# Kernel optimization log

Hardware: AMD Instinct MI355X
Metric: run time of the kernel (lower is better)

Reference implementation:

```python
import jax, jax.numpy as jnp
import numpy as np

B, N, IN_CH = 4, 8192, 4
K = 16
W0, W1, W2 = 64, 128, 256
NUM_CLASSES = 3


def setup_inputs() -> dict:
    key = jax.random.key(0)
    ks = jax.random.split(key, 16)

    def lin(kw, kb, fan_in, fan_out):
        bound = 1.0 / np.sqrt(fan_in)
        w = jax.random.uniform(kw, (fan_in, fan_out), jnp.float32, -bound, bound)
        b = jax.random.uniform(kb, (fan_out,), jnp.float32, -bound, bound)
        return w, b

    x = jax.random.normal(ks[0], (B, N, IN_CH), jnp.float32)
    stem_w, stem_b = lin(ks[1], ks[2], IN_CH, W0)
    b1_w, b1_b = lin(ks[3], ks[4], 2 * W0 + 3, W1)
    b2_w, b2_b = lin(ks[5], ks[6], 2 * W1 + 3, W2)
    glob_w, glob_b = lin(ks[7], ks[8], W2, W2)
    head1_w, head1_b = lin(ks[9], ks[10], 2 * W2, W2)
    head2_w, head2_b = lin(ks[11], ks[12], W2, NUM_CLASSES)
    return {
        'x': x,
        'hmix_a': jnp.float32(1.0), 'hmix_b': jnp.float32(1.0), 'hmix_c': jnp.float32(0.0),
        'stem_w': stem_w, 'stem_b': stem_b,
        'b1_w': b1_w, 'b1_b': b1_b,
        'b2_w': b2_w, 'b2_b': b2_b,
        'glob_w': glob_w, 'glob_b': glob_b,
        'head1_w': head1_w, 'head1_b': head1_b,
        'head2_w': head2_w, 'head2_b': head2_b,
        'thresh': jnp.float32(0.15), 'sharp': jnp.float32(10.0), 'scale': jnp.float32(0.5),
    }


def _knn_idx(coords, k):
    # coords: [B,N,3] -> idx of k nearest neighbors (incl. self), no grad.
    c = jax.lax.stop_gradient(coords)
    xx = jnp.sum(c * c, axis=-1, keepdims=True)            # [B,N,1]
    dist = xx + jnp.swapaxes(xx, 1, 2) - 2.0 * jnp.einsum('bnc,bmc->bnm', c, c)
    dist = jnp.maximum(dist, 0.0)
    _, idx = jax.lax.top_k(-dist, k)                       # smallest distances
    return idx                                             # [B,N,k]


def _local_agg(coords, feat, idx, w, b):
    # gather-concat-MLP-maxpool, faithful to LocalAggBlock (pool='max')
    bidx = jnp.arange(coords.shape[0])[:, None, None]
    nb_f = feat[bidx, idx]                                 # [B,N,k,C]
    nb_p = coords[bidx, idx]                               # [B,N,k,3]
    fi = feat[:, :, None, :]
    pi = coords[:, :, None, :]
    h = jnp.concatenate(
        [jnp.broadcast_to(fi, nb_f.shape), nb_f - fi, nb_p - pi], axis=-1)
    h = jax.nn.relu(jnp.einsum('bnkd,do->bnko', h, w) + b)
    return jnp.max(h, axis=2)                              # [B,N,out]


def reference(x, hmix_a, hmix_b, hmix_c, stem_w, stem_b, b1_w, b1_b,
              b2_w, b2_b, glob_w, glob_b, head1_w, head1_b,
              head2_w, head2_b, thresh, sharp, scale):
    # HeightMixer: z_eff = a*z + b*hag + c
    z_eff = hmix_a * x[..., 2] + hmix_b * x[..., 3] + hmix_c
    coords = jnp.stack([x[..., 0], x[..., 1], z_eff], axis=-1)  # [B,N,3]

    f = jax.nn.relu(x @ stem_w + stem_b)                   # stem: [B,N,64]

    # both blocks use the same coords -> same KNN graph; compute once
    idx = _knn_idx(coords, K)
    f = _local_agg(coords, f, idx, b1_w, b1_b)             # [B,N,128]
    f = _local_agg(coords, f, idx, b2_w, b2_b)             # [B,N,256]

    g = jnp.max(f, axis=1)                                 # [B,256]
    g = jax.nn.relu(g @ glob_w + glob_b)
    g = jnp.broadcast_to(g[:, None, :], f.shape)           # [B,N,256]

    h = jnp.concatenate([f, g], axis=-1)                   # [B,N,512]
    h = jax.nn.relu(h @ head1_w + head1_b)
    logits = h @ head2_w + head2_b                         # [B,N,3]

    # HeightPriorBias on class 0
    hag = x[..., 3]
    bias = scale * jax.nn.sigmoid(sharp * (thresh - hag))
    logits = logits.at[..., 0].add(bias)
    return logits
```

## Files before the change

### kernel.cpp

```cpp
#include <hip/hip_runtime.h>
#include <math.h>

typedef unsigned long long u64;
typedef unsigned int u32;
typedef _Float16 h8v __attribute__((ext_vector_type(8)));
typedef float    f4v __attribute__((ext_vector_type(4)));
typedef float    f2v __attribute__((ext_vector_type(2)));

#define MFMA16(a,b,c) __builtin_amdgcn_mfma_f32_16x16x32_f16(a, b, c, 0, 0, 0)

#define B_ 4
#define N_ 8192
#define K_ 16
#define W0_ 64
#define W1_ 128
#define W2_ 256
#define X0_ 96
#define X1_ 160

__global__ __launch_bounds__(256) void prep_kernel(
    const float* __restrict__ x,
    const float* __restrict__ stem_w, const float* __restrict__ stem_b,
    const float* __restrict__ hmix_a, const float* __restrict__ hmix_b,
    const float* __restrict__ hmix_c,
    float* __restrict__ coords4, _Float16* __restrict__ fx0,
    _Float16* __restrict__ fx1) {
  const int p = blockIdx.x * 4 + (threadIdx.x >> 6);
  const int o = threadIdx.x & 63;
  const float x0 = x[p*4+0], x1 = x[p*4+1], x2 = x[p*4+2], x3 = x[p*4+3];
  const float z = hmix_a[0]*x2 + hmix_b[0]*x3 + hmix_c[0];
  float acc = stem_b[o] + x0*stem_w[0*W0_+o] + x1*stem_w[1*W0_+o]
            + x2*stem_w[2*W0_+o] + x3*stem_w[3*W0_+o];
  fx0[p*X0_+o] = (_Float16)fmaxf(acc, 0.f);
  if (o < 32) {
    const float tv = (o==0) ? x0 : (o==1) ? x1 : (o==2) ? z : 0.f;
    fx0[p*X0_+W0_+o] = (_Float16)tv;
    fx1[(size_t)p*X1_+W1_+o] = (_Float16)tv;
  }
  if (o == 0) {
    const float xx = x0*x0 + x1*x1 + z*z;
    ((float4*)coords4)[p] = make_float4(x0, x1, z, xx);
  }
}

template<int DIN, int DOUT, int XDIM>
__global__ void wconv_kernel(const float* __restrict__ w,
    _Float16* __restrict__ midT, _Float16* __restrict__ difT) {
  const int o = blockIdx.x;
  const int c = threadIdx.x;
  float mv = 0.f, dv = 0.f;
  if (c < DIN)        { const float wm = w[(DIN+c)*DOUT+o]; mv = wm; dv = w[c*DOUT+o] - wm; }
  else if (c < DIN+3) { const float wp = w[(2*DIN+(c-DIN))*DOUT+o]; mv = wp; dv = -wp; }
  midT[o*XDIM+c] = (_Float16)mv;
  difT[o*XDIM+c] = (_Float16)dv;
}

__global__ __launch_bounds__(256) void htrans_kernel(
    const float* __restrict__ h1w, _Float16* __restrict__ h1wT) {
  const int o = blockIdx.x;
  for (int c = threadIdx.x; c < 512; c += 256)
    h1wT[(size_t)o*512 + c] = (_Float16)h1w[(size_t)c*256 + o];
}

#define DPP_SHR1(v) __builtin_amdgcn_update_dpp(0, (v), 0x138, 0xF, 0xF, false)

#define DPP_MIN(v, ctrl)                                                        \
  { const int _t = __builtin_amdgcn_update_dpp(__float_as_int(v),               \
      __float_as_int(v), ctrl, 0xF, 0xF, false);                                \
    v = fminf(v, __int_as_float(_t)); }

__device__ __forceinline__ float sixteenth_of_minima(float v) {
  float th = 0.f;
#pragma unroll
  for (int r = 0; r < 16; ++r) {
    float w = v;
    DPP_MIN(w, 0x111); DPP_MIN(w, 0x112); DPP_MIN(w, 0x114); DPP_MIN(w, 0x118);
    DPP_MIN(w, 0x142); DPP_MIN(w, 0x143);
    const float mv = __int_as_float(
        __builtin_amdgcn_readlane(__float_as_int(w), 63));
    th = mv;
    v = (v == mv) ? INFINITY : v;
  }
  return th;
}

#define KNN_EVT(d, dk, ik)                                                      \
  {                                                                             \
    const int s = (int)__ffsll((unsigned long long)m) - 1;  m &= m - 1;         \
    const float dc = __int_as_float(__builtin_amdgcn_readlane(                  \
                       __float_as_int(d), s));                                  \
    const bool cnd = dc < dk;                                                   \
    const u64 cm = __ballot(cnd) << 1;                                          \
    const float pd = __int_as_float(DPP_SHR1(__float_as_int(dk)));              \
    const int   pi = DPP_SHR1(ik);                                              \
    const bool pc = (cm >> lane) & 1;                                           \
    dk = cnd ? (pc ? pd : dc) : dk;                                             \
    ik = cnd ? (pc ? pi : (jbase + s)) : ik;                                    \
  }

#define KNN_CHUNK(d, dk, ik, T, Th)                                             \
  { u64 m = __ballot(d <= T);                                                   \
    if (m) {                                                                    \
      do { KNN_EVT(d, dk, ik) } while (m);                                      \
      T = fminf(Th, __int_as_float(__builtin_amdgcn_readlane(                   \
            __float_as_int(dk), 15)));                                          \
    }                                                                           \
  }

#define KNN_DIST2(dA, dB)                                                       \
  const f2v cjx = {cj.x, cj.x}, cjy = {cj.y, cj.y},                             \
            cjz = {cj.z, cj.z}, cjw = {cj.w, cj.w};                             \
  f2v tA = cAx * cjx;                                                           \
  tA = __builtin_elementwise_fma(cAy, cjy, tA);                                 \
  tA = __builtin_elementwise_fma(cAz, cjz, tA);                                 \
  const f2v dA = __builtin_elementwise_fma(tA, m2, cAw + cjw);                  \
  f2v tB = cBx * cjx;                                                           \
  tB = __builtin_elementwise_fma(cBy, cjy, tB);                                 \
  tB = __builtin_elementwise_fma(cBz, cjz, tB);                                 \
  const f2v dB = __builtin_elementwise_fma(tB, m2, cBw + cjw);

__global__ __launch_bounds__(256, 8) void knn_kernel(
    const float* __restrict__ coords4, int* __restrict__ knn_idx) {
  const int tid = threadIdx.x;
  const int wid = tid >> 6;
  const int lane = tid & 63;
  const int p0 = blockIdx.x * 16 + wid * 4;
  const int b = p0 >> 13;
  const float4* cb = ((const float4*)coords4) + (b << 13);
  const float4 c0 = ((const float4*)coords4)[p0+0];
  const float4 c1 = ((const float4*)coords4)[p0+1];
  const float4 c2 = ((const float4*)coords4)[p0+2];
  const float4 c3 = ((const float4*)coords4)[p0+3];
  const f2v m2 = {-2.f, -2.f};
  const f2v cAx = {c0.x, c1.x}, cAy = {c0.y, c1.y}, cAz = {c0.z, c1.z}, cAw = {c0.w, c1.w};
  const f2v cBx = {c2.x, c3.x}, cBy = {c2.y, c3.y}, cBz = {c2.z, c3.z}, cBw = {c2.w, c3.w};

  float lm0 = INFINITY, lm1 = INFINITY, lm2 = INFINITY, lm3 = INFINITY;
  for (int it = 0; it < 64; ++it) {
    const float4 cj = cb[it*64 + lane];
    KNN_DIST2(dA, dB)
    lm0 = fminf(lm0, fmaxf(dA[0], 0.f));
    lm1 = fminf(lm1, fmaxf(dA[1], 0.f));
    lm2 = fminf(lm2, fmaxf(dB[0], 0.f));
    lm3 = fminf(lm3, fmaxf(dB[1], 0.f));
  }
  const float Th0 = sixteenth_of_minima(lm0);
  const float Th1 = sixteenth_of_minima(lm1);
  const float Th2 = sixteenth_of_minima(lm2);
  const float Th3 = sixteenth_of_minima(lm3);

  float dk0 = INFINITY, dk1 = INFINITY, dk2 = INFINITY, dk3 = INFINITY;
  int   ik0 = 0, ik1 = 0, ik2 = 0, ik3 = 0;
  float T0 = Th0, T1 = Th1, T2 = Th2, T3 = Th3;

  for (int it = 0; it < N_/64; ++it) {
    const int jbase = it*64;
    const float4 cj = cb[jbase + lane];
    KNN_DIST2(dA, dB)
    const float d0 = fmaxf(dA[0], 0.f);
    const float d1 = fmaxf(dA[1], 0.f);
    const float d2 = fmaxf(dB[0], 0.f);
    const float d3 = fmaxf(dB[1], 0.f);
    KNN_CHUNK(d0, dk0, ik0, T0, Th0);
    KNN_CHUNK(d1, dk1, ik1, T1, Th1);
    KNN_CHUNK(d2, dk2, ik2, T2, Th2);
    KNN_CHUNK(d3, dk3, ik3, T3, Th3);
  }

  if (lane < K_) {
    knn_idx[(size_t)(p0+0)*K_ + lane] = ik0;
    knn_idx[(size_t)(p0+1)*K_ + lane] = ik1;
    knn_idx[(size_t)(p0+2)*K_ + lane] = ik2;
    knn_idx[(size_t)(p0+3)*K_ + lane] = ik3;
  }
}

template<int KS, int NPASS>
__global__ __launch_bounds__(256) void aggm_kernel(
    const _Float16* __restrict__ fx, const int* __restrict__ knn_idx,
    const _Float16* __restrict__ midT, const _Float16* __restrict__ difT,
    const float* __restrict__ bw,
    _Float16* __restrict__ fo, const int ostr) {
  const int XD  = KS*32;
  const int XDP = XD + 8;
  const int CH  = KS*4;
  const int p0 = blockIdx.x * 16;
  const int bb = (p0 >> 13) << 13;
  const int tid = threadIdx.x;
  const int w = tid >> 6, lane = tid & 63, col = lane & 15, quad = lane >> 4;
  const int koff = quad * 8;

  __shared__ int s_idx[256];
  __shared__ _Float16 sA[2][16*(KS*32+8)];

  s_idx[tid] = knn_idx[p0*K_ + tid];

  f4v cacc[NPASS][2];
  {
    h8v Ao[KS];
    const _Float16* ap = fx + (size_t)(p0+col)*XD + koff;
#pragma unroll
    for (int kk = 0; kk < KS; ++kk) Ao[kk] = *(const h8v*)(ap + kk*32);
#pragma unroll
    for (int ps = 0; ps < NPASS; ++ps) {
      const int o0 = ps*128 + w*32;
      const _Float16* b0 = difT + (size_t)(o0 + col)*XD + koff;
      const _Float16* b1 = difT + (size_t)(o0 + 16 + col)*XD + koff;
      f4v c0 = {0.f,0.f,0.f,0.f}, c1 = {0.f,0.f,0.f,0.f};
#pragma unroll
      for (int kk = 0; kk < KS; ++kk) {
        c0 = MFMA16(Ao[kk], *(const h8v*)(b0 + kk*32), c0);
        c1 = MFMA16(Ao[kk], *(const h8v*)(b1 + kk*32), c1);
      }
      cacc[ps][0] = c0; cacc[ps][1] = c1;
    }
  }

  h8v Bf[NPASS][2][KS];
  float bias[NPASS][2];
#pragma unroll
  for (int ps = 0; ps < NPASS; ++ps) {
    const int o0 = ps*128 + w*32;
#pragma unroll
    for (int kk = 0; kk < KS; ++kk) {
      Bf[ps][0][kk] = *(const h8v*)(midT + (size_t)(o0 + col)*XD + kk*32 + koff);
      Bf[ps][1][kk] = *(const h8v*)(midT + (size_t)(o0 + 16 + col)*XD + kk*32 + koff);
    }
    bias[ps][0] = bw[o0 + col];
    bias[ps][1] = bw[o0 + 16 + col];
  }
  __syncthreads();

  for (int c = tid; c < 16*CH; c += 256) {
    const int r = c / CH, o = c - r*CH;
    *(uint4*)&sA[0][r*XDP + o*8] =
        *(const uint4*)(fx + (size_t)(bb + s_idx[r<<4])*XD + o*8);
  }
  __syncthreads();

  f4v M[NPASS][2];
#pragma unroll
  for (int ps = 0; ps < NPASS; ++ps) {
    M[ps][0] = (f4v){-INFINITY,-INFINITY,-INFINITY,-INFINITY};
    M[ps][1] = (f4v){-INFINITY,-INFINITY,-INFINITY,-INFINITY};
  }

  for (int k = 0; k < 16; ++k) {
    const int buf = k & 1;
    if (k < 15) {
      for (int c = tid; c < 16*CH; c += 256) {
        const int r = c / CH, o = c - r*CH;
        *(uint4*)&sA[buf^1][r*XDP + o*8] =
            *(const uint4*)(fx + (size_t)(bb + s_idx[(r<<4) + k + 1])*XD + o*8);
      }
    }
    h8v Ac[KS];
    const _Float16* ap = &sA[buf][col*XDP + koff];
#pragma unroll
    for (int kk = 0; kk < KS; ++kk) Ac[kk] = *(const h8v*)(ap + kk*32);
#pragma unroll
    for (int ps = 0; ps < NPASS; ++ps) {
      f4v d0 = {0.f,0.f,0.f,0.f}, d1 = {0.f,0.f,0.f,0.f};
#pragma unroll
      for (int kk = 0; kk < KS; ++kk) {
        d0 = MFMA16(Ac[kk], Bf[ps][0][kk], d0);
        d1 = MFMA16(Ac[kk], Bf[ps][1][kk], d1);
      }
#pragma unroll
      for (int e = 0; e < 4; ++e) {
        M[ps][0][e] = fmaxf(M[ps][0][e], d0[e]);
        M[ps][1][e] = fmaxf(M[ps][1][e], d1[e]);
      }
    }
    __syncthreads();
  }

  const int prow = p0 + (quad << 2);
#pragma unroll
  for (int ps = 0; ps < NPASS; ++ps) {
    const int o0 = ps*128 + w*32;
    const int oa = o0 + col, ob = oa + 16;
#pragma unroll
    for (int reg = 0; reg < 4; ++reg) {
      fo[(size_t)(prow+reg)*ostr + oa] =
          (_Float16)fmaxf(M[ps][0][reg] + cacc[ps][0][reg] + bias[ps][0], 0.f);
      fo[(size_t)(prow+reg)*ostr + ob] =
          (_Float16)fmaxf(M[ps][1][reg] + cacc[ps][1][reg] + bias[ps][1], 0.f);
    }
  }
}

__global__ __launch_bounds__(256) void gmax_kernel(
    const _Float16* __restrict__ f2h, float* __restrict__ part) {
  const int b = blockIdx.x >> 5;
  const int seg = blockIdx.x & 31;
  const int tid = threadIdx.x;
  const int rg = tid >> 5;
  const int cc = (tid & 31) * 8;
  __shared__ float smax[8][256];
  const size_t rbase = (size_t)(b << 13) + seg*256;
  _Float16 mh[8];
#pragma unroll
  for (int j = 0; j < 8; ++j) mh[j] = (_Float16)0.f;
  for (int n = rg; n < 256; n += 8) {
    const h8v v = *(const h8v*)&f2h[(rbase + n)*W2_ + cc];
#pragma unroll
    for (int j = 0; j < 8; ++j) mh[j] = (v[j] > mh[j]) ? v[j] : mh[j];
  }
#pragma unroll
  for (int j = 0; j < 8; ++j) smax[rg][cc + j] = (float)mh[j];
  __syncthreads();
  float m = smax[0][tid];
#pragma unroll
  for (int g = 1; g < 8; ++g) m = fmaxf(m, smax[g][tid]);
  part[(size_t)blockIdx.x*W2_ + tid] = m;
}

__global__ __launch_bounds__(256) void gfc_kernel(
    const float* __restrict__ part, const float* __restrict__ gw,
    const float* __restrict__ gb, _Float16* __restrict__ g2h) {
  const int b = blockIdx.x;
  const int o = threadIdx.x;
  __shared__ float s_g[W2_];
  float m = -INFINITY;
  for (int s = 0; s < 32; ++s) m = fmaxf(m, part[(size_t)(b*32+s)*W2_ + o]);
  s_g[o] = m;
  __syncthreads();
  float acc = gb[o];
  for (int d = 0; d < W2_; ++d) acc += s_g[d]*gw[d*W2_ + o];
  g2h[b*W2_ + o] = (_Float16)fmaxf(acc, 0.f);
}

__global__ __launch_bounds__(256) void headm_kernel(
    const _Float16* __restrict__ f2h, const _Float16* __restrict__ g2h,
    const _Float16* __restrict__ h1wT, const float* __restrict__ h1b,
    const float* __restrict__ h2w, const float* __restrict__ h2b,
    const float* __restrict__ x,
    const float* __restrict__ thresh, const float* __restrict__ sharp,
    const float* __restrict__ scale,
    float* __restrict__ out) {
  const int p0 = blockIdx.x * 32;
  const int b = p0 >> 13;
  const int tid = threadIdx.x;
  const int w = tid >> 6, lane = tid & 63, col = lane & 15, quad = lane >> 4;

  __shared__ _Float16 sA[32*520];
  __shared__ float    sh[32*260];

  for (int t = tid; t < 32*32; t += 256) {
    const int r = t >> 5, cc = (t & 31) * 8;
    *(uint4*)&sA[r*520 + cc] = *(const uint4*)&f2h[(size_t)(p0+r)*W2_ + cc];
  }
  for (int t = tid; t < 32*32; t += 256) {
    const int r = t >> 5, cc = (t & 31) * 8;
    *(uint4*)&sA[r*520 + 256 + cc] = *(const uint4*)&g2h[b*W2_ + cc];
  }
  __syncthreads();

  f4v acc[2][4];
#pragma unroll
  for (int r = 0; r < 2; ++r)
#pragma unroll
    for (int t = 0; t < 4; ++t) acc[r][t] = (f4v){0.f,0.f,0.f,0.f};

  for (int kk = 0; kk < 16; ++kk) {
    const h8v a0 = *(const h8v*)&sA[col*520 + kk*32 + quad*8];
    const h8v a1 = *(const h8v*)&sA[(16+col)*520 + kk*32 + quad*8];
#pragma unroll
    for (int t = 0; t < 4; ++t) {
      const h8v bt = *(const h8v*)&h1wT[(size_t)(w*64 + t*16 + col)*512 + kk*32 + quad*8];
      acc[0][t] = MFMA16(a0, bt, acc[0][t]);
      acc[1][t] = MFMA16(a1, bt, acc[1][t]);
    }
  }
#pragma unroll
  for (int r = 0; r < 2; ++r)
#pragma unroll
    for (int t = 0; t < 4; ++t) {
      const int o = w*64 + t*16 + col;
      const float bv = h1b[o];
#pragma unroll
      for (int reg = 0; reg < 4; ++reg)
        sh[(r*16 + quad*4 + reg)*260 + o] = fmaxf(acc[r][t][reg] + bv, 0.f);
    }
  __syncthreads();

  if (tid < 96) {
    const int pp = tid / 3, c = tid % 3;
    float s = h2b[c];
    for (int d = 0; d < 256; ++d) s += sh[pp*260 + d] * h2w[d*3 + c];
    if (c == 0) {
      const float hag = x[(size_t)(p0+pp)*4 + 3];
      s += scale[0] / (1.f + expf(-sharp[0]*(thresh[0] - hag)));
    }
    out[(size_t)(p0+pp)*3 + c] = s;
  }
}

extern "C" void kernel_launch(void* const* d_in, const int* in_sizes, int n_in,
                              void* d_out, int out_size, void* d_ws, size_t ws_size,
                              hipStream_t stream) {
  const float* x       = (const float*)d_in[0];
  const float* hmix_a  = (const float*)d_in[1];
  const float* hmix_b  = (const float*)d_in[2];
  const float* hmix_c  = (const float*)d_in[3];
  const float* stem_w  = (const float*)d_in[4];
  const float* stem_b  = (const float*)d_in[5];
  const float* b1_w    = (const float*)d_in[6];
  const float* b1_b    = (const float*)d_in[7];
  const float* b2_w    = (const float*)d_in[8];
  const float* b2_b    = (const float*)d_in[9];
  const float* glob_w  = (const float*)d_in[10];
  const float* glob_b  = (const float*)d_in[11];
  const float* head1_w = (const float*)d_in[12];
  const float* head1_b = (const float*)d_in[13];
  const float* head2_w = (const float*)d_in[14];
  const float* head2_b = (const float*)d_in[15];
  const float* thresh  = (const float*)d_in[16];
  const float* sharp   = (const float*)d_in[17];
  const float* scale   = (const float*)d_in[18];
  float* out = (float*)d_out;

  char* base = (char*)d_ws;
  float*     coords4 = (float*)    (base + 0);
  int*       idxb    = (int*)      (base + 524288);
  _Float16*  fx0     = (_Float16*) (base + 2621440);
  _Float16*  fx1     = (_Float16*) (base + 8912896);
  _Float16*  f2h     = (_Float16*) (base + 19398656);
  _Float16*  w1m     = (_Float16*) (base + 36175872);
  _Float16*  w1d     = (_Float16*) (base + 36200448);
  _Float16*  w2m     = (_Float16*) (base + 36225024);
  _Float16*  w2d     = (_Float16*) (base + 36306944);
  _Float16*  h1wT    = (_Float16*) (base + 36388864);
  float*     part    = (float*)    (base + 36651008);
  _Float16*  g2h     = (_Float16*) (base + 36782080);

  const int NP = B_ * N_;

  wconv_kernel<W0_, W1_, X0_><<<W1_, X0_, 0, stream>>>(b1_w, w1m, w1d);
  wconv_kernel<W1_, W2_, X1_><<<W2_, X1_, 0, stream>>>(b2_w, w2m, w2d);
  htrans_kernel<<<W2_, 256, 0, stream>>>(head1_w, h1wT);
  prep_kernel<<<NP/4, 256, 0, stream>>>(x, stem_w, stem_b, hmix_a, hmix_b, hmix_c,
                                        coords4, fx0, fx1);
  knn_kernel<<<NP/16, 256, 0, stream>>>(coords4, idxb);
  aggm_kernel<3, 1><<<NP/16, 256, 0, stream>>>(fx0, idxb, w1m, w1d, b1_b, fx1, X1_);
  aggm_kernel<5, 2><<<NP/16, 256, 0, stream>>>(fx1, idxb, w2m, w2d, b2_b, f2h, W2_);
  gmax_kernel<<<B_*32, 256, 0, stream>>>(f2h, part);
  gfc_kernel<<<B_, 256, 0, stream>>>(part, glob_w, glob_b, g2h);
  headm_kernel<<<NP/32, 256, 0, stream>>>(f2h, g2h, h1wT, head1_b, head2_w, head2_b,
                                          x, thresh, sharp, scale, out);
}
```

Baseline: 453.8 us.

## Fuse weight prep into prep kernel and global max into second aggregation

The three weight-conversion/transposition kernels are folded into the prep kernel as extra blocks, which removes launches. The separate global-max kernel is dropped: the second aggregation kernel now reduces each block's post-ReLU outputs across lanes and writes them with unsigned-int atomicMax into a per-batch buffer that a memset zeroes first. gfc then reads that buffer directly. This saves launches and a full re-read of the 256-wide feature tensor, but adds global atomics and a memset call. The uint max is valid only because the values are non-negative after ReLU.

```diff
diff --git a/kernel.cpp b/kernel.cpp
--- a/kernel.cpp
+++ b/kernel.cpp
@@ -24,42 +24,55 @@
     const float* __restrict__ hmix_a, const float* __restrict__ hmix_b,
     const float* __restrict__ hmix_c,
     float* __restrict__ coords4, _Float16* __restrict__ fx0,
-    _Float16* __restrict__ fx1) {
-  const int p = blockIdx.x * 4 + (threadIdx.x >> 6);
-  const int o = threadIdx.x & 63;
-  const float x0 = x[p*4+0], x1 = x[p*4+1], x2 = x[p*4+2], x3 = x[p*4+3];
-  const float z = hmix_a[0]*x2 + hmix_b[0]*x3 + hmix_c[0];
-  float acc = stem_b[o] + x0*stem_w[0*W0_+o] + x1*stem_w[1*W0_+o]
-            + x2*stem_w[2*W0_+o] + x3*stem_w[3*W0_+o];
-  fx0[p*X0_+o] = (_Float16)fmaxf(acc, 0.f);
-  if (o < 32) {
-    const float tv = (o==0) ? x0 : (o==1) ? x1 : (o==2) ? z : 0.f;
-    fx0[p*X0_+W0_+o] = (_Float16)tv;
-    fx1[(size_t)p*X1_+W1_+o] = (_Float16)tv;
-  }
-  if (o == 0) {
-    const float xx = x0*x0 + x1*x1 + z*z;
-    ((float4*)coords4)[p] = make_float4(x0, x1, z, xx);
-  }
-}
-
-template<int DIN, int DOUT, int XDIM>
-__global__ void wconv_kernel(const float* __restrict__ w,
-    _Float16* __restrict__ midT, _Float16* __restrict__ difT) {
-  const int o = blockIdx.x;
-  const int c = threadIdx.x;
-  float mv = 0.f, dv = 0.f;
-  if (c < DIN)        { const float wm = w[(DIN+c)*DOUT+o]; mv = wm; dv = w[c*DOUT+o] - wm; }
-  else if (c < DIN+3) { const float wp = w[(2*DIN+(c-DIN))*DOUT+o]; mv = wp; dv = -wp; }
-  midT[o*XDIM+c] = (_Float16)mv;
-  difT[o*XDIM+c] = (_Float16)dv;
-}
-
-__global__ __launch_bounds__(256) void htrans_kernel(
-    const float* __restrict__ h1w, _Float16* __restrict__ h1wT) {
-  const int o = blockIdx.x;
-  for (int c = threadIdx.x; c < 512; c += 256)
-    h1wT[(size_t)o*512 + c] = (_Float16)h1w[(size_t)c*256 + o];
+    _Float16* __restrict__ fx1,
+    const float* __restrict__ b1_w, const float* __restrict__ b2_w,
+    const float* __restrict__ h1w,
+    _Float16* __restrict__ w1m, _Float16* __restrict__ w1d,
+    _Float16* __restrict__ w2m, _Float16* __restrict__ w2d,
+    _Float16* __restrict__ h1wT) {
+  const int bi = blockIdx.x;
+  const int tid = threadIdx.x;
+  const int PB = (B_*N_)/4;
+  if (bi < PB) {
+    const int p = bi * 4 + (tid >> 6);
+    const int o = tid & 63;
+    const float x0 = x[p*4+0], x1 = x[p*4+1], x2 = x[p*4+2], x3 = x[p*4+3];
+    const float z = hmix_a[0]*x2 + hmix_b[0]*x3 + hmix_c[0];
+    float acc = stem_b[o] + x0*stem_w[0*W0_+o] + x1*stem_w[1*W0_+o]
+              + x2*stem_w[2*W0_+o] + x3*stem_w[3*W0_+o];
+    fx0[p*X0_+o] = (_Float16)fmaxf(acc, 0.f);
+    if (o < 32) {
+      const float tv = (o==0) ? x0 : (o==1) ? x1 : (o==2) ? z : 0.f;
+      fx0[p*X0_+W0_+o] = (_Float16)tv;
+      fx1[(size_t)p*X1_+W1_+o] = (_Float16)tv;
+    }
+    if (o == 0) {
+      const float xx = x0*x0 + x1*x1 + z*z;
+      ((float4*)coords4)[p] = make_float4(x0, x1, z, xx);
+    }
+  } else if (bi < PB + W1_) {
+    const int o = bi - PB, c = tid;
+    if (c < X0_) {
+      float mv = 0.f, dv = 0.f;
+      if (c < W0_)        { const float wm = b1_w[(W0_+c)*W1_+o]; mv = wm; dv = b1_w[c*W1_+o] - wm; }
+      else if (c < W0_+3) { const float wp = b1_w[(2*W0_+(c-W0_))*W1_+o]; mv = wp; dv = -wp; }
+      w1m[o*X0_+c] = (_Float16)mv;
+      w1d[o*X0_+c] = (_Float16)dv;
+    }
+  } else if (bi < PB + W1_ + W2_) {
+    const int o = bi - PB - W1_, c = tid;
+    if (c < X1_) {
+      float mv = 0.f, dv = 0.f;
+      if (c < W1_)        { const float wm = b2_w[(W1_+c)*W2_+o]; mv = wm; dv = b2_w[c*W2_+o] - wm; }
+      else if (c < W1_+3) { const float wp = b2_w[(2*W1_+(c-W1_))*W2_+o]; mv = wp; dv = -wp; }
+      w2m[o*X1_+c] = (_Float16)mv;
+      w2d[o*X1_+c] = (_Float16)dv;
+    }
+  } else {
+    const int o = bi - PB - W1_ - W2_;
+    for (int c = tid; c < 512; c += 256)
+      h1wT[(size_t)o*512 + c] = (_Float16)h1w[(size_t)c*256 + o];
+  }
 }
 
 #define DPP_SHR1(v) __builtin_amdgcn_update_dpp(0, (v), 0x138, 0xF, 0xF, false)
@@ -175,12 +188,12 @@
   }
 }
 
-template<int KS, int NPASS>
+template<int KS, int NPASS, bool GMAX>
 __global__ __launch_bounds__(256) void aggm_kernel(
     const _Float16* __restrict__ fx, const int* __restrict__ knn_idx,
     const _Float16* __restrict__ midT, const _Float16* __restrict__ difT,
     const float* __restrict__ bw,
-    _Float16* __restrict__ fo, const int ostr) {
+    _Float16* __restrict__ fo, const int ostr, u32* __restrict__ part) {
   const int XD  = KS*32;
   const int XDP = XD + 8;
   const int CH  = KS*4;
@@ -276,44 +289,32 @@
   }
 
   const int prow = p0 + (quad << 2);
+  const int bq = p0 >> 13;
 #pragma unroll
   for (int ps = 0; ps < NPASS; ++ps) {
     const int o0 = ps*128 + w*32;
     const int oa = o0 + col, ob = oa + 16;
+    float v0[4], v1[4];
 #pragma unroll
     for (int reg = 0; reg < 4; ++reg) {
-      fo[(size_t)(prow+reg)*ostr + oa] =
-          (_Float16)fmaxf(M[ps][0][reg] + cacc[ps][0][reg] + bias[ps][0], 0.f);
-      fo[(size_t)(prow+reg)*ostr + ob] =
-          (_Float16)fmaxf(M[ps][1][reg] + cacc[ps][1][reg] + bias[ps][1], 0.f);
-    }
-  }
-}
-
-__global__ __launch_bounds__(256) void gmax_kernel(
-    const _Float16* __restrict__ f2h, float* __restrict__ part) {
-  const int b = blockIdx.x >> 5;
-  const int seg = blockIdx.x & 31;
-  const int tid = threadIdx.x;
-  const int rg = tid >> 5;
-  const int cc = (tid & 31) * 8;
-  __shared__ float smax[8][256];
-  const size_t rbase = (size_t)(b << 13) + seg*256;
-  _Float16 mh[8];
-#pragma unroll
-  for (int j = 0; j < 8; ++j) mh[j] = (_Float16)0.f;
-  for (int n = rg; n < 256; n += 8) {
-    const h8v v = *(const h8v*)&f2h[(rbase + n)*W2_ + cc];
-#pragma unroll
-    for (int j = 0; j < 8; ++j) mh[j] = (v[j] > mh[j]) ? v[j] : mh[j];
-  }
-#pragma unroll
-  for (int j = 0; j < 8; ++j) smax[rg][cc + j] = (float)mh[j];
-  __syncthreads();
-  float m = smax[0][tid];
-#pragma unroll
-  for (int g = 1; g < 8; ++g) m = fmaxf(m, smax[g][tid]);
-  part[(size_t)blockIdx.x*W2_ + tid] = m;
+      v0[reg] = fmaxf(M[ps][0][reg] + cacc[ps][0][reg] + bias[ps][0], 0.f);
+      v1[reg] = fmaxf(M[ps][1][reg] + cacc[ps][1][reg] + bias[ps][1], 0.f);
+      fo[(size_t)(prow+reg)*ostr + oa] = (_Float16)v0[reg];
+      fo[(size_t)(prow+reg)*ostr + ob] = (_Float16)v1[reg];
+    }
+    if (GMAX) {
+      float bm0 = fmaxf(fmaxf(v0[0], v0[1]), fmaxf(v0[2], v0[3]));
+      float bm1 = fmaxf(fmaxf(v1[0], v1[1]), fmaxf(v1[2], v1[3]));
+      bm0 = fmaxf(bm0, __shfl_xor(bm0, 16, 64));
+      bm0 = fmaxf(bm0, __shfl_xor(bm0, 32, 64));
+      bm1 = fmaxf(bm1, __shfl_xor(bm1, 16, 64));
+      bm1 = fmaxf(bm1, __shfl_xor(bm1, 32, 64));
+      if (quad == 0) {
+        atomicMax(part + bq*W2_ + oa, __float_as_uint(bm0));
+        atomicMax(part + bq*W2_ + ob, __float_as_uint(bm1));
+      }
+    }
+  }
 }
 
 __global__ __launch_bounds__(256) void gfc_kernel(
@@ -322,9 +323,7 @@
   const int b = blockIdx.x;
   const int o = threadIdx.x;
   __shared__ float s_g[W2_];
-  float m = -INFINITY;
-  for (int s = 0; s < 32; ++s) m = fmaxf(m, part[(size_t)(b*32+s)*W2_ + o]);
-  s_g[o] = m;
+  s_g[o] = part[b*W2_ + o];
   __syncthreads();
   float acc = gb[o];
   for (int d = 0; d < W2_; ++d) acc += s_g[d]*gw[d*W2_ + o];
@@ -437,15 +436,15 @@
 
   const int NP = B_ * N_;
 
-  wconv_kernel<W0_, W1_, X0_><<<W1_, X0_, 0, stream>>>(b1_w, w1m, w1d);
-  wconv_kernel<W1_, W2_, X1_><<<W2_, X1_, 0, stream>>>(b2_w, w2m, w2d);
-  htrans_kernel<<<W2_, 256, 0, stream>>>(head1_w, h1wT);
-  prep_kernel<<<NP/4, 256, 0, stream>>>(x, stem_w, stem_b, hmix_a, hmix_b, hmix_c,
-                                        coords4, fx0, fx1);
+  prep_kernel<<<NP/4 + W1_ + 2*W2_, 256, 0, stream>>>(
+      x, stem_w, stem_b, hmix_a, hmix_b, hmix_c, coords4, fx0, fx1,
+      b1_w, b2_w, head1_w, w1m, w1d, w2m, w2d, h1wT);
+  hipMemsetAsync(part, 0, B_*W2_*sizeof(float), stream);
   knn_kernel<<<NP/16, 256, 0, stream>>>(coords4, idxb);
-  aggm_kernel<3, 1><<<NP/16, 256, 0, stream>>>(fx0, idxb, w1m, w1d, b1_b, fx1, X1_);
-  aggm_kernel<5, 2><<<NP/16, 256, 0, stream>>>(fx1, idxb, w2m, w2d, b2_b, f2h, W2_);
-  gmax_kernel<<<B_*32, 256, 0, stream>>>(f2h, part);
+  aggm_kernel<3, 1, false><<<NP/16, 256, 0, stream>>>(
+      fx0, idxb, w1m, w1d, b1_b, fx1, X1_, (u32*)0);
+  aggm_kernel<5, 2, true><<<NP/16, 256, 0, stream>>>(
+      fx1, idxb, w2m, w2d, b2_b, f2h, W2_, (u32*)part);
   gfc_kernel<<<B_, 256, 0, stream>>>(part, glob_w, glob_b, g2h);
   headm_kernel<<<NP/32, 256, 0, stream>>>(f2h, g2h, h1wT, head1_b, head2_w, head2_b,
                                           x, thresh, sharp, scale, out);
```

After: 445.1 us. No clear change (-1.9%).
